# Optimization experiments

Hardware: AMD Instinct MI355X
Metric: run time of the kernel (lower is better)

The kernel has to match this reference:

```python
import jax, jax.numpy as jnp
import numpy as np

N, F, H, T = 100000, 128, 128, 10
E = 1600000
NUM_GRAPHS = 512
BN_EPS = 1e-5


def setup_inputs() -> dict:
    key = jax.random.key(0)
    ks = jax.random.split(key, 16)
    x = jax.random.normal(ks[0], (N, F), dtype=jnp.float32)
    edge_index = jax.random.randint(ks[1], (2, E), 0, N, dtype=jnp.int64)
    batch = jnp.sort(jax.random.randint(ks[2], (N,), 0, NUM_GRAPHS, dtype=jnp.int64))
    s = lambda fin: 1.0 / np.sqrt(fin)
    return {
        "x": x, "edge_index": edge_index, "batch": batch,
        # GINConv 1 MLP: Linear(F,H) -> BN(H) -> ReLU -> Linear(H,H)
        "W1a": jax.random.uniform(ks[3], (F, H), jnp.float32, -s(F), s(F)),
        "b1a": jax.random.uniform(ks[4], (H,), jnp.float32, -s(F), s(F)),
        "g1": jnp.ones((H,), jnp.float32),
        "bt1": jnp.zeros((H,), jnp.float32),
        "W1b": jax.random.uniform(ks[5], (H, H), jnp.float32, -s(H), s(H)),
        "b1b": jax.random.uniform(ks[6], (H,), jnp.float32, -s(H), s(H)),
        # GINConv 2 MLP
        "W2a": jax.random.uniform(ks[7], (H, H), jnp.float32, -s(H), s(H)),
        "b2a": jax.random.uniform(ks[8], (H,), jnp.float32, -s(H), s(H)),
        "g2": jnp.ones((H,), jnp.float32),
        "bt2": jnp.zeros((H,), jnp.float32),
        "W2b": jax.random.uniform(ks[9], (H, H), jnp.float32, -s(H), s(H)),
        "b2b": jax.random.uniform(ks[10], (H,), jnp.float32, -s(H), s(H)),
        # final Linear(H, T)
        "Wl": jax.random.uniform(ks[11], (H, T), jnp.float32, -s(H), s(H)),
        "bl": jax.random.uniform(ks[12], (T,), jnp.float32, -s(H), s(H)),
    }


def _batchnorm(h, gamma, beta):
    # training-mode BN over the node dimension (biased variance), eps=1e-5
    mean = jnp.mean(h, axis=0)
    var = jnp.mean(jnp.square(h - mean), axis=0)
    return (h - mean) * jax.lax.rsqrt(var + BN_EPS) * gamma + beta


def _gin_conv(x, edge_index, Wa, ba, gamma, beta, Wb, bb):
    src, dst = edge_index[0], edge_index[1]
    # sum-aggregate neighbor messages: scatter-add x[src] into dst rows
    agg = jax.ops.segment_sum(x[src], dst, num_segments=x.shape[0])
    h = (x + agg) @ Wa + ba          # eps=0 in GINConv default
    h = jax.nn.relu(_batchnorm(h, gamma, beta))
    return h @ Wb + bb


def reference(x, edge_index, batch, W1a, b1a, g1, bt1, W1b, b1b,
              W2a, b2a, g2, bt2, W2b, b2b, Wl, bl):
    h = jax.nn.relu(_gin_conv(x, edge_index, W1a, b1a, g1, bt1, W1b, b1b))
    h = jax.nn.relu(_gin_conv(h, edge_index, W2a, b2a, g2, bt2, W2b, b2b))
    pooled = jax.ops.segment_sum(h, batch, num_segments=NUM_GRAPHS)  # [G, H]
    return pooled @ Wl + bl  # [G, T]
```

## Files before the change

kernel.cpp:

```cpp
#include <hip/hip_runtime.h>
#include <cstdint>
#include <cstddef>

#define NFEAT 128
#define TGRAPH 10
#define NGRAPHS 512
#define BN_EPS 1e-5f
#define BIN_CHUNK 2048
#define GSPAN 8
#define TSTR 24

typedef __attribute__((ext_vector_type(8))) short bf16x8;
typedef __attribute__((ext_vector_type(4))) float f32x4;
typedef __attribute__((ext_vector_type(2))) float f32x2;

__device__ __forceinline__ float bf2f(short s) {
    union { unsigned u; float f; } c;
    c.u = ((unsigned)(unsigned short)s) << 16;
    return c.f;
}
__device__ __forceinline__ short f2bf(float f) {
    union { float f; unsigned u; } c;
    c.f = f;
    unsigned u = c.u;
    return (short)((u + 0x7fffu + ((u >> 16) & 1u)) >> 16);
}
__device__ __forceinline__ unsigned cvt_pk_bf16(float lo, float hi) {
    unsigned r;
    asm("v_cvt_pk_bf16_f32 %0, %1, %2" : "=v"(r) : "v"(lo), "v"(hi));
    return r;
}
__device__ __forceinline__ void accp(f32x2& a, unsigned v) {
    union { unsigned u; float f; } lo, hi;
    lo.u = v << 16;
    hi.u = v & 0xffff0000u;
    f32x2 t;
    t[0] = lo.f;
    t[1] = hi.f;
    a += t;
}


__global__ void k_bucket_scan(const int* __restrict__ bhist, int* __restrict__ bbase,
                              int* __restrict__ cur256, int E) {
    __shared__ int s[256];
    int t = threadIdx.x;
    int v = bhist[t];
    s[t] = v;
    __syncthreads();
    for (int off = 1; off < 256; off <<= 1) {
        int x = 0;
        if (t >= off) x = s[t - off];
        __syncthreads();
        if (t >= off) s[t] += x;
        __syncthreads();
    }
    int excl = s[t] - v;
    bbase[t] = excl;
    cur256[t] = excl;
    if (t == 255) bbase[256] = E;
}

__global__ __launch_bounds__(256) void k_bin_scatter(const int* __restrict__ src,
                                                     const int* __restrict__ dst,
                                                     int* __restrict__ cur256,
                                                     int2* __restrict__ binned, int E) {
    __shared__ int hist[256];
    __shared__ int base[256];
    int t = threadIdx.x;
    int e0 = blockIdx.x * BIN_CHUNK;
    int e1 = min(e0 + BIN_CHUNK, E);
    hist[t] = 0;
    __syncthreads();
    for (int e = e0 + t; e < e1; e += 256) {
        int b = dst[e] >> 9;
        atomicAdd(&hist[b], 1);
    }
    __syncthreads();
    int c = hist[t];
    if (c > 0) base[t] = atomicAdd(&cur256[t], c);
    __syncthreads();
    hist[t] = 0;
    __syncthreads();
    for (int e = e0 + t; e < e1; e += 256) {
        int d = dst[e];
        int b = d >> 9;
        int loc = atomicAdd(&hist[b], 1);
        binned[base[b] + loc] = make_int2(src[e], d);
    }
}

__global__ __launch_bounds__(512) void k_bucket_csr(const int2* __restrict__ binned,
                                                    const int* __restrict__ bbase,
                                                    int* __restrict__ rowptr,
                                                    int* __restrict__ adj,
                                                    int N, int E, int nb) {
    __shared__ int deg[512];
    __shared__ int cur[512];
    int b = blockIdx.x;
    int t = threadIdx.x;
    int e0 = bbase[b], e1 = bbase[b + 1];
    deg[t] = 0;
    __syncthreads();
    for (int e = e0 + t; e < e1; e += 512)
        atomicAdd(&deg[binned[e].y & 511], 1);
    __syncthreads();
    int v = deg[t];
    for (int off = 1; off < 512; off <<= 1) {
        int x = 0;
        if (t >= off) x = deg[t - off];
        __syncthreads();
        if (t >= off) deg[t] += x;
        __syncthreads();
    }
    int excl = deg[t] - v;
    cur[t] = excl;
    int node = b * 512 + t;
    if (node < N) rowptr[node] = e0 + excl;
    if (b == nb - 1 && t == 0) rowptr[N] = E;
    __syncthreads();
    for (int e = e0 + t; e < e1; e += 512) {
        int2 p = binned[e];
        int loc = atomicAdd(&cur[p.y & 511], 1);
        adj[e0 + loc] = p.x;
    }
}

__global__ __launch_bounds__(256) void k_prep_hist(const int* __restrict__ dst,
                                                   int* __restrict__ bhist, int E, int hb,
                                                   const float* __restrict__ x,
                                                   short* __restrict__ xbf,
                                                   const float* __restrict__ W0,
                                                   const float* __restrict__ W1,
                                                   const float* __restrict__ W2,
                                                   const float* __restrict__ W3,
                                                   short* __restrict__ Wf, int n4) {
    int t = threadIdx.x;
    if (blockIdx.x < hb) {
        __shared__ int h[256];
        h[t] = 0;
        __syncthreads();
        for (int e = blockIdx.x * 256 + t; e < E; e += hb * 256)
            atomicAdd(&h[dst[e] >> 9], 1);
        __syncthreads();
        if (h[t]) atomicAdd(&bhist[t], h[t]);
        return;
    }
    int i = (blockIdx.x - hb) * 256 + t;
    if (i < n4) {
        float4 v = ((const float4*)x)[i];
        uint2 o;
        o.x = cvt_pk_bf16(v.x, v.y);
        o.y = cvt_pk_bf16(v.z, v.w);
        ((uint2*)xbf)[i] = o;
    } else {
        int idx = i - n4;
        if (idx < 4 * 16384) {
            int w = idx >> 14, r = idx & 16383;
            int j = r & 7, lane = (r >> 3) & 63, ct = (r >> 9) & 7, kc = r >> 12;
            int k = kc * 32 + (lane >> 4) * 8 + j;
            int n = ct * 16 + (lane & 15);
            const float* W = (w == 0) ? W0 : (w == 1) ? W1 : (w == 2) ? W2 : W3;
            Wf[idx] = f2bf(W[k * NFEAT + n]);
        }
    }
}

__global__ __launch_bounds__(256) void k_aggregate_v4(const short* __restrict__ X,
                                                      const int* __restrict__ rowptr,
                                                      const int* __restrict__ adj,
                                                      short* __restrict__ XA, int N) {
    int tid = threadIdx.x;
    int lane = tid & 63;
    int g = lane >> 4;
    int p = lane & 15;
    int wid = (blockIdx.x * blockDim.x + tid) >> 6;
    if (wid >= N) return;
    const uint4* Xv = (const uint4*)X;
    f32x2 ac[4];
#pragma unroll
    for (int j = 0; j < 4; j++) ac[j] = (f32x2){0.f, 0.f};
    int r0 = rowptr[wid], r1 = rowptr[wid + 1];
    for (int e = r0; e < r1; e += 16) {
        int ea = e + g, eb = e + 4 + g, ec = e + 8 + g, ed = e + 12 + g;
        uint4 v0 = {0u, 0u, 0u, 0u}, v1 = {0u, 0u, 0u, 0u};
        uint4 v2 = {0u, 0u, 0u, 0u}, v3 = {0u, 0u, 0u, 0u};
        if (ea < r1) v0 = Xv[(size_t)adj[ea] * 16 + p];
        if (eb < r1) v1 = Xv[(size_t)adj[eb] * 16 + p];
        if (ec < r1) v2 = Xv[(size_t)adj[ec] * 16 + p];
        if (ed < r1) v3 = Xv[(size_t)adj[ed] * 16 + p];
        accp(ac[0], v0.x); accp(ac[1], v0.y); accp(ac[2], v0.z); accp(ac[3], v0.w);
        accp(ac[0], v1.x); accp(ac[1], v1.y); accp(ac[2], v1.z); accp(ac[3], v1.w);
        accp(ac[0], v2.x); accp(ac[1], v2.y); accp(ac[2], v2.z); accp(ac[3], v2.w);
        accp(ac[0], v3.x); accp(ac[1], v3.y); accp(ac[2], v3.z); accp(ac[3], v3.w);
    }
#pragma unroll
    for (int j = 0; j < 4; j++) {
        ac[j][0] += __shfl_xor(ac[j][0], 16);
        ac[j][1] += __shfl_xor(ac[j][1], 16);
        ac[j][0] += __shfl_xor(ac[j][0], 32);
        ac[j][1] += __shfl_xor(ac[j][1], 32);
    }
    if (g == 0) {
        uint4 sv = Xv[(size_t)wid * 16 + p];
        accp(ac[0], sv.x); accp(ac[1], sv.y); accp(ac[2], sv.z); accp(ac[3], sv.w);
        uint4 o;
        o.x = cvt_pk_bf16(ac[0][0], ac[0][1]);
        o.y = cvt_pk_bf16(ac[1][0], ac[1][1]);
        o.z = cvt_pk_bf16(ac[2][0], ac[2][1]);
        o.w = cvt_pk_bf16(ac[3][0], ac[3][1]);
        size_t dst = ((size_t)(wid >> 4) * 4 + (p >> 2)) * 512 +
                     (size_t)(((p & 3) * 16 + (wid & 15)) * 8);
        *(uint4*)(XA + dst) = o;
    }
}

template <bool BN_RELU_IN, bool RELU_OUT, bool STATS, bool FRAG_OUT, bool POOL>
__global__ __launch_bounds__(256) void k_gemm_mfma(const short* __restrict__ A,
                                                   const short* __restrict__ Wf,
                                                   const float* __restrict__ bias,
                                                   float* __restrict__ stats,
                                                   const float* __restrict__ gamma,
                                                   const float* __restrict__ beta,
                                                   const int* __restrict__ batch,
                                                   float* __restrict__ pooled,
                                                   short* __restrict__ C, int N) {
    __shared__ float s_aux[256];
    __shared__ __align__(16) short c_tile[4][32 * TSTR];
    __shared__ float s_pool[GSPAN][NFEAT];
    int tid = threadIdx.x;
    int wave = tid >> 6, lane = tid & 63;
    int quad = lane >> 4, l16 = lane & 15;
    int row_base = blockIdx.x * 128 + wave * 32;

    int gbase = 0;
    if constexpr (POOL) {
        int first = blockIdx.x * 128;
        gbase = (first < N) ? batch[first] : 0;
        for (int i = tid; i < GSPAN * NFEAT; i += 256) s_pool[i >> 7][i & 127] = 0.f;
    }
    if constexpr (STATS) s_aux[tid] = 0.f;
    if constexpr (BN_RELU_IN) {
        if (tid < NFEAT) {
            float mean = stats[tid] / (float)N;
            float var = stats[NFEAT + tid] / (float)N - mean * mean;
            float inv = rsqrtf(var + BN_EPS);
            float sc = gamma[tid] * inv;
            s_aux[tid] = sc;
            s_aux[NFEAT + tid] = beta[tid] - mean * sc;
        }
    }
    if constexpr (STATS || BN_RELU_IN || POOL) __syncthreads();

    f32x4 acc[2][8];
#pragma unroll
    for (int i = 0; i < 2; i++)
#pragma unroll
        for (int j = 0; j < 8; j++) acc[i][j] = (f32x4){0.f, 0.f, 0.f, 0.f};

    const short* af = A + ((size_t)(blockIdx.x * 8 + wave * 2) * 4) * 512;

#pragma unroll
    for (int kc = 0; kc < 4; ++kc) {
        bf16x8 a0 = *(const bf16x8*)(af + (size_t)kc * 512 + lane * 8);
        bf16x8 a1 = *(const bf16x8*)(af + (size_t)(4 + kc) * 512 + lane * 8);
        if constexpr (BN_RELU_IN) {
            int koff = kc * 32 + quad * 8;
            union { bf16x8 v; unsigned u[4]; } r0, r1;
#pragma unroll
            for (int h = 0; h < 4; ++h) {
                float sca = s_aux[koff + 2 * h];
                float scb = s_aux[koff + 2 * h + 1];
                float sha = s_aux[NFEAT + koff + 2 * h];
                float shb = s_aux[NFEAT + koff + 2 * h + 1];
                float x0 = fmaxf(bf2f(a0[2 * h]) * sca + sha, 0.f);
                float x1 = fmaxf(bf2f(a0[2 * h + 1]) * scb + shb, 0.f);
                float y0 = fmaxf(bf2f(a1[2 * h]) * sca + sha, 0.f);
                float y1 = fmaxf(bf2f(a1[2 * h + 1]) * scb + shb, 0.f);
                r0.u[h] = cvt_pk_bf16(x0, x1);
                r1.u[h] = cvt_pk_bf16(y0, y1);
            }
            a0 = r0.v;
            a1 = r1.v;
        }
        const short* wp = Wf + ((size_t)(kc * 8) * 64 + lane) * 8;
#pragma unroll
        for (int ct = 0; ct < 8; ++ct) {
            bf16x8 b = *(const bf16x8*)(wp + (size_t)ct * 64 * 8);
            acc[0][ct] = __builtin_amdgcn_mfma_f32_16x16x32_bf16(a0, b, acc[0][ct], 0, 0, 0);
            acc[1][ct] = __builtin_amdgcn_mfma_f32_16x16x32_bf16(a1, b, acc[1][ct], 0, 0, 0);
        }
    }

    int dg[8];
    if constexpr (POOL) {
#pragma unroll
        for (int rt = 0; rt < 2; ++rt)
#pragma unroll
            for (int reg = 0; reg < 4; ++reg) {
                int row = row_base + rt * 16 + quad * 4 + reg;
                dg[rt * 4 + reg] = (row < N) ? (batch[row] - gbase) : -1;
            }
    }

    short* tile = &c_tile[wave][0];
    int row2 = lane >> 1, half = lane & 1;
#pragma unroll
    for (int ct = 0; ct < 8; ++ct) {
        int col = ct * 16 + l16;
        float bv = bias[col];
        float ls = 0.f, ls2 = 0.f;
        int cg = -1;
        float ps = 0.f;
#pragma unroll
        for (int rt = 0; rt < 2; ++rt) {
            float v[4];
#pragma unroll
            for (int reg = 0; reg < 4; ++reg) {
                int lrow = rt * 16 + quad * 4 + reg;
                float x = acc[rt][ct][reg] + bv;
                if constexpr (RELU_OUT) x = fmaxf(x, 0.f);
                if constexpr (STATS) {
                    if (row_base + lrow < N) { ls += x; ls2 += x * x; }
                }
                if constexpr (POOL) {
                    int d = dg[rt * 4 + reg];
                    if (d != cg) {
                        if (cg >= 0) atomicAdd(&s_pool[cg & (GSPAN - 1)][col], ps);
                        cg = d; ps = 0.f;
                    }
                    if (d >= 0) ps += x;
                }
                v[reg] = x;
            }
            if constexpr (!POOL) {
                unsigned p01 = cvt_pk_bf16(v[0], v[1]);
                unsigned p23 = cvt_pk_bf16(v[2], v[3]);
                int lr = rt * 16 + quad * 4;
                tile[lr * TSTR + l16] = (short)p01;
                tile[(lr + 1) * TSTR + l16] = (short)(p01 >> 16);
                tile[(lr + 2) * TSTR + l16] = (short)p23;
                tile[(lr + 3) * TSTR + l16] = (short)(p23 >> 16);
            }
        }
        if constexpr (POOL) {
            if (cg >= 0) atomicAdd(&s_pool[cg & (GSPAN - 1)][col], ps);
        }
        if constexpr (STATS) {
            ls += __shfl_xor(ls, 16);
            ls += __shfl_xor(ls, 32);
            ls2 += __shfl_xor(ls2, 16);
            ls2 += __shfl_xor(ls2, 32);
            if (quad == 0) {
                atomicAdd(&s_aux[col], ls);
                atomicAdd(&s_aux[NFEAT + col], ls2);
            }
        }
        if constexpr (!POOL) {
            uint4 val = *(const uint4*)(tile + row2 * TSTR + half * 8);
            int grow = row_base + row2;
            if (grow < N) {
                int col0 = ct * 16 + half * 8;
                if constexpr (FRAG_OUT) {
                    size_t addr = ((size_t)(grow >> 4) * 4 + (col0 >> 5)) * 512 +
                                  (size_t)((((col0 >> 3) & 3) * 16 + (grow & 15)) * 8);
                    *(uint4*)(C + addr) = val;
                } else {
                    *(uint4*)(C + (size_t)grow * NFEAT + col0) = val;
                }
            }
        }
    }

    if constexpr (STATS) {
        __syncthreads();
        if (tid < NFEAT) {
            atomicAdd(&stats[tid], s_aux[tid]);
            atomicAdd(&stats[NFEAT + tid], s_aux[NFEAT + tid]);
        }
    }
    if constexpr (POOL) {
        __syncthreads();
        for (int i = tid; i < GSPAN * NFEAT; i += 256) {
            float v = s_pool[i >> 7][i & 127];
            if (v != 0.f) {
                int gg = gbase + (i >> 7);
                if (gg < NGRAPHS) atomicAdd(&pooled[gg * NFEAT + (i & 127)], v);
            }
        }
    }
}

__global__ void k_final(const float* __restrict__ pooled, const float* __restrict__ Wl,
                        const float* __restrict__ bl, float* __restrict__ out) {
    int idx = blockIdx.x * blockDim.x + threadIdx.x;
    if (idx >= NGRAPHS * TGRAPH) return;
    int g = idx / TGRAPH, t = idx % TGRAPH;
    const float* p = pooled + (size_t)g * NFEAT;
    float acc = bl[t];
#pragma unroll 16
    for (int k = 0; k < NFEAT; ++k) acc += p[k] * Wl[k * TGRAPH + t];
    out[idx] = acc;
}

extern "C" void kernel_launch(void* const* d_in, const int* in_sizes, int n_in,
                              void* d_out, int out_size, void* d_ws, size_t ws_size,
                              hipStream_t stream) {
    const float* x = (const float*)d_in[0];
    const int* ei = (const int*)d_in[1];
    const int* batch = (const int*)d_in[2];
    const float* W1a = (const float*)d_in[3];
    const float* b1a = (const float*)d_in[4];
    const float* g1 = (const float*)d_in[5];
    const float* bt1 = (const float*)d_in[6];
    const float* W1b = (const float*)d_in[7];
    const float* b1b = (const float*)d_in[8];
    const float* W2a = (const float*)d_in[9];
    const float* b2a = (const float*)d_in[10];
    const float* g2 = (const float*)d_in[11];
    const float* bt2 = (const float*)d_in[12];
    const float* W2b = (const float*)d_in[13];
    const float* b2b = (const float*)d_in[14];
    const float* Wl = (const float*)d_in[15];
    const float* bl = (const float*)d_in[16];
    float* out = (float*)d_out;

    int N = in_sizes[2];
    int E = in_sizes[1] / 2;
    int nb = (N + 511) >> 9;
    const int* src = ei;
    const int* dst = ei + E;

    int gemmBlocks = (N + 127) / 128;
    int padRows = gemmBlocks * 128;

    char* ws = (char*)d_ws;
    size_t off = 0;
    auto alloc = [&](size_t bytes) -> void* {
        void* p = ws + off;
        off = (off + bytes + 255) & ~(size_t)255;
        return p;
    };
    short* xbf = (short*)alloc((size_t)N * NFEAT * 2);
    short* ag = (short*)alloc((size_t)padRows * NFEAT * 2);
    short* ybf = (short*)alloc((size_t)padRows * NFEAT * 2);
    short* hbf = (short*)alloc((size_t)N * NFEAT * 2);
    short* Wf = (short*)alloc((size_t)4 * 16384 * 2);
    int* adj = (int*)alloc((size_t)E * 4);
    int2* binned = (int2*)alloc((size_t)E * 8);
    int* rowptr = (int*)alloc((size_t)(N + 1) * 4);
    int* bbase = (int*)alloc(257 * 4);
    int* cur256 = (int*)alloc(256 * 4);
    int* bhist = (int*)alloc(256 * 4);
    float* stats1 = (float*)alloc(256 * 4);
    float* stats2 = (float*)alloc(256 * 4);
    float* pooled = (float*)alloc((size_t)NGRAPHS * NFEAT * 4);
    size_t zbytes = (char*)(pooled + (size_t)NGRAPHS * NFEAT) - (char*)bhist;

    hipMemsetAsync(bhist, 0, zbytes, stream);

    int n4 = N * NFEAT / 4;
    int prepTot = n4 + 4 * 16384;
    int hb = 784;
    k_prep_hist<<<hb + (prepTot + 255) / 256, 256, 0, stream>>>(
        dst, bhist, E, hb, x, xbf, W1a, W1b, W2a, W2b, Wf, n4);
    k_bucket_scan<<<1, 256, 0, stream>>>(bhist, bbase, cur256, E);
    k_bin_scatter<<<(E + BIN_CHUNK - 1) / BIN_CHUNK, 256, 0, stream>>>(src, dst, cur256, binned, E);
    k_bucket_csr<<<nb, 512, 0, stream>>>(binned, bbase, rowptr, adj, N, E, nb);

    int aggBlocks = (N + 3) / 4;

    k_aggregate_v4<<<aggBlocks, 256, 0, stream>>>(xbf, rowptr, adj, ag, N);
    k_gemm_mfma<false, false, true, true, false><<<gemmBlocks, 256, 0, stream>>>(
        ag, Wf + 0 * 16384, b1a, stats1, nullptr, nullptr, nullptr, nullptr, ybf, N);
    k_gemm_mfma<true, true, false, false, false><<<gemmBlocks, 256, 0, stream>>>(
        ybf, Wf + 1 * 16384, b1b, stats1, g1, bt1, nullptr, nullptr, hbf, N);

    k_aggregate_v4<<<aggBlocks, 256, 0, stream>>>(hbf, rowptr, adj, ag, N);
    k_gemm_mfma<false, false, true, true, false><<<gemmBlocks, 256, 0, stream>>>(
        ag, Wf + 2 * 16384, b2a, stats2, nullptr, nullptr, nullptr, nullptr, ybf, N);
    k_gemm_mfma<true, true, false, false, true><<<gemmBlocks, 256, 0, stream>>>(
        ybf, Wf + 3 * 16384, b2b, stats2, g2, bt2, batch, pooled, nullptr, N);

    k_final<<<(NGRAPHS * TGRAPH + 255) / 256, 256, 0, stream>>>(pooled, Wl, bl, out);
}
```

Baseline: 449.5 us.

## Fuse both GIN MLP GEMMs into one persistent kernel with grid barrier

The two GEMMs of each GIN MLP, split before by the BatchNorm statistics dependency, now run in one persistent kernel sized to occupancy. A software grid barrier on an atomic counter sits between the two phases. Each block keeps its first 128-row intermediate tile in LDS, so part of the Y write and reread through global memory is skipped, and one launch per layer is removed. The cost is a spin barrier that deadlocks if not all blocks are co-resident, extra LDS use that limits occupancy, and fewer blocks each looping over several tiles.

```diff
diff --git a/kernel.cpp b/kernel.cpp
--- a/kernel.cpp
+++ b/kernel.cpp
@@ -215,125 +215,69 @@
     }
 }
 
-template <bool BN_RELU_IN, bool RELU_OUT, bool STATS, bool FRAG_OUT, bool POOL>
-__global__ __launch_bounds__(256) void k_gemm_mfma(const short* __restrict__ A,
-                                                   const short* __restrict__ Wf,
-                                                   const float* __restrict__ bias,
-                                                   float* __restrict__ stats,
-                                                   const float* __restrict__ gamma,
-                                                   const float* __restrict__ beta,
-                                                   const int* __restrict__ batch,
-                                                   float* __restrict__ pooled,
-                                                   short* __restrict__ C, int N) {
+template <bool POOLB>
+__global__ __launch_bounds__(256, 3) void k_gemm_fused(
+    const short* __restrict__ A, const short* __restrict__ Wa,
+    const short* __restrict__ Wb, const float* __restrict__ ba,
+    const float* __restrict__ bb, float* __restrict__ stats,
+    const float* __restrict__ gamma, const float* __restrict__ beta,
+    const int* __restrict__ batch, float* __restrict__ pooled,
+    short* __restrict__ Y, short* __restrict__ C,
+    int* __restrict__ bar, int nTiles, int N) {
     __shared__ float s_aux[256];
+    __shared__ __align__(16) short ylds[16384];
     __shared__ __align__(16) short c_tile[4][32 * TSTR];
     __shared__ float s_pool[GSPAN][NFEAT];
     int tid = threadIdx.x;
     int wave = tid >> 6, lane = tid & 63;
     int quad = lane >> 4, l16 = lane & 15;
-    int row_base = blockIdx.x * 128 + wave * 32;
-
-    int gbase = 0;
-    if constexpr (POOL) {
-        int first = blockIdx.x * 128;
-        gbase = (first < N) ? batch[first] : 0;
-        for (int i = tid; i < GSPAN * NFEAT; i += 256) s_pool[i >> 7][i & 127] = 0.f;
-    }
-    if constexpr (STATS) s_aux[tid] = 0.f;
-    if constexpr (BN_RELU_IN) {
-        if (tid < NFEAT) {
-            float mean = stats[tid] / (float)N;
-            float var = stats[NFEAT + tid] / (float)N - mean * mean;
-            float inv = rsqrtf(var + BN_EPS);
-            float sc = gamma[tid] * inv;
-            s_aux[tid] = sc;
-            s_aux[NFEAT + tid] = beta[tid] - mean * sc;
-        }
-    }
-    if constexpr (STATS || BN_RELU_IN || POOL) __syncthreads();
-
-    f32x4 acc[2][8];
-#pragma unroll
-    for (int i = 0; i < 2; i++)
-#pragma unroll
-        for (int j = 0; j < 8; j++) acc[i][j] = (f32x4){0.f, 0.f, 0.f, 0.f};
-
-    const short* af = A + ((size_t)(blockIdx.x * 8 + wave * 2) * 4) * 512;
-
-#pragma unroll
-    for (int kc = 0; kc < 4; ++kc) {
-        bf16x8 a0 = *(const bf16x8*)(af + (size_t)kc * 512 + lane * 8);
-        bf16x8 a1 = *(const bf16x8*)(af + (size_t)(4 + kc) * 512 + lane * 8);
-        if constexpr (BN_RELU_IN) {
-            int koff = kc * 32 + quad * 8;
-            union { bf16x8 v; unsigned u[4]; } r0, r1;
-#pragma unroll
-            for (int h = 0; h < 4; ++h) {
-                float sca = s_aux[koff + 2 * h];
-                float scb = s_aux[koff + 2 * h + 1];
-                float sha = s_aux[NFEAT + koff + 2 * h];
-                float shb = s_aux[NFEAT + koff + 2 * h + 1];
-                float x0 = fmaxf(bf2f(a0[2 * h]) * sca + sha, 0.f);
-                float x1 = fmaxf(bf2f(a0[2 * h + 1]) * scb + shb, 0.f);
-                float y0 = fmaxf(bf2f(a1[2 * h]) * sca + sha, 0.f);
-                float y1 = fmaxf(bf2f(a1[2 * h + 1]) * scb + shb, 0.f);
-                r0.u[h] = cvt_pk_bf16(x0, x1);
-                r1.u[h] = cvt_pk_bf16(y0, y1);
-            }
-            a0 = r0.v;
-            a1 = r1.v;
-        }
-        const short* wp = Wf + ((size_t)(kc * 8) * 64 + lane) * 8;
+    int row2 = lane >> 1, half = lane & 1;
+
+    bool lds0 = true;
+    for (int t = blockIdx.x; t < nTiles; t += gridDim.x, lds0 = false) {
+        int row_base = t * 128 + wave * 32;
+        const short* af = A + ((size_t)(t * 8 + wave * 2) * 4) * 512;
+        bf16x8 a0[4], a1[4];
+#pragma unroll
+        for (int kc = 0; kc < 4; ++kc) {
+            a0[kc] = *(const bf16x8*)(af + (size_t)kc * 512 + lane * 8);
+            a1[kc] = *(const bf16x8*)(af + (size_t)(4 + kc) * 512 + lane * 8);
+        }
+        s_aux[tid] = 0.f;
+        __syncthreads();
+
+        f32x4 acc[2][8];
+#pragma unroll
+        for (int i = 0; i < 2; i++)
+#pragma unroll
+            for (int j = 0; j < 8; j++) acc[i][j] = (f32x4){0.f, 0.f, 0.f, 0.f};
+#pragma unroll
+        for (int kc = 0; kc < 4; ++kc) {
+            const short* wp = Wa + ((size_t)(kc * 8) * 64 + lane) * 8;
+#pragma unroll
+            for (int ct = 0; ct < 8; ++ct) {
+                bf16x8 b = *(const bf16x8*)(wp + (size_t)ct * 64 * 8);
+                acc[0][ct] = __builtin_amdgcn_mfma_f32_16x16x32_bf16(a0[kc], b, acc[0][ct], 0, 0, 0);
+                acc[1][ct] = __builtin_amdgcn_mfma_f32_16x16x32_bf16(a1[kc], b, acc[1][ct], 0, 0, 0);
+            }
+        }
+
+        short* tile = &c_tile[wave][0];
 #pragma unroll
         for (int ct = 0; ct < 8; ++ct) {
-            bf16x8 b = *(const bf16x8*)(wp + (size_t)ct * 64 * 8);
-            acc[0][ct] = __builtin_amdgcn_mfma_f32_16x16x32_bf16(a0, b, acc[0][ct], 0, 0, 0);
-            acc[1][ct] = __builtin_amdgcn_mfma_f32_16x16x32_bf16(a1, b, acc[1][ct], 0, 0, 0);
-        }
-    }
-
-    int dg[8];
-    if constexpr (POOL) {
-#pragma unroll
-        for (int rt = 0; rt < 2; ++rt)
-#pragma unroll
-            for (int reg = 0; reg < 4; ++reg) {
-                int row = row_base + rt * 16 + quad * 4 + reg;
-                dg[rt * 4 + reg] = (row < N) ? (batch[row] - gbase) : -1;
-            }
-    }
-
-    short* tile = &c_tile[wave][0];
-    int row2 = lane >> 1, half = lane & 1;
-#pragma unroll
-    for (int ct = 0; ct < 8; ++ct) {
-        int col = ct * 16 + l16;
-        float bv = bias[col];
-        float ls = 0.f, ls2 = 0.f;
-        int cg = -1;
-        float ps = 0.f;
-#pragma unroll
-        for (int rt = 0; rt < 2; ++rt) {
-            float v[4];
-#pragma unroll
-            for (int reg = 0; reg < 4; ++reg) {
-                int lrow = rt * 16 + quad * 4 + reg;
-                float x = acc[rt][ct][reg] + bv;
-                if constexpr (RELU_OUT) x = fmaxf(x, 0.f);
-                if constexpr (STATS) {
+            int col = ct * 16 + l16;
+            float bv = ba[col];
+            float ls = 0.f, ls2 = 0.f;
+#pragma unroll
+            for (int rt = 0; rt < 2; ++rt) {
+                float v[4];
+#pragma unroll
+                for (int reg = 0; reg < 4; ++reg) {
+                    int lrow = rt * 16 + quad * 4 + reg;
+                    float x = acc[rt][ct][reg] + bv;
                     if (row_base + lrow < N) { ls += x; ls2 += x * x; }
+                    v[reg] = x;
                 }
-                if constexpr (POOL) {
-                    int d = dg[rt * 4 + reg];
-                    if (d != cg) {
-                        if (cg >= 0) atomicAdd(&s_pool[cg & (GSPAN - 1)][col], ps);
-                        cg = d; ps = 0.f;
-                    }
-                    if (d >= 0) ps += x;
-                }
-                v[reg] = x;
-            }
-            if constexpr (!POOL) {
                 unsigned p01 = cvt_pk_bf16(v[0], v[1]);
                 unsigned p23 = cvt_pk_bf16(v[2], v[3]);
                 int lr = rt * 16 + quad * 4;
@@ -342,11 +286,6 @@
                 tile[(lr + 2) * TSTR + l16] = (short)p23;
                 tile[(lr + 3) * TSTR + l16] = (short)(p23 >> 16);
             }
-        }
-        if constexpr (POOL) {
-            if (cg >= 0) atomicAdd(&s_pool[cg & (GSPAN - 1)][col], ps);
-        }
-        if constexpr (STATS) {
             ls += __shfl_xor(ls, 16);
             ls += __shfl_xor(ls, 32);
             ls2 += __shfl_xor(ls2, 16);
@@ -355,37 +294,168 @@
                 atomicAdd(&s_aux[col], ls);
                 atomicAdd(&s_aux[NFEAT + col], ls2);
             }
-        }
-        if constexpr (!POOL) {
             uint4 val = *(const uint4*)(tile + row2 * TSTR + half * 8);
-            int grow = row_base + row2;
-            if (grow < N) {
-                int col0 = ct * 16 + half * 8;
-                if constexpr (FRAG_OUT) {
-                    size_t addr = ((size_t)(grow >> 4) * 4 + (col0 >> 5)) * 512 +
-                                  (size_t)((((col0 >> 3) & 3) * 16 + (grow & 15)) * 8);
-                    *(uint4*)(C + addr) = val;
-                } else {
-                    *(uint4*)(C + (size_t)grow * NFEAT + col0) = val;
-                }
-            }
-        }
-    }
-
-    if constexpr (STATS) {
+            int lrow2 = wave * 32 + row2;
+            int col0 = ct * 16 + half * 8;
+            size_t fa = ((size_t)(lrow2 >> 4) * 4 + (col0 >> 5)) * 512 +
+                        (size_t)((((col0 >> 3) & 3) * 16 + (lrow2 & 15)) * 8);
+            if (lds0) {
+                *(uint4*)(ylds + fa) = val;
+            } else {
+                int grow = row_base + row2;
+                if (grow < N) *(uint4*)(Y + (size_t)t * 16384 + fa) = val;
+            }
+        }
         __syncthreads();
         if (tid < NFEAT) {
             atomicAdd(&stats[tid], s_aux[tid]);
             atomicAdd(&stats[NFEAT + tid], s_aux[NFEAT + tid]);
         }
-    }
-    if constexpr (POOL) {
-        __syncthreads();
-        for (int i = tid; i < GSPAN * NFEAT; i += 256) {
-            float v = s_pool[i >> 7][i & 127];
-            if (v != 0.f) {
-                int gg = gbase + (i >> 7);
-                if (gg < NGRAPHS) atomicAdd(&pooled[gg * NFEAT + (i & 127)], v);
+        __syncthreads();
+    }
+
+    __threadfence();
+    __syncthreads();
+    if (tid == 0) {
+        __hip_atomic_fetch_add(bar, 1, __ATOMIC_RELEASE, __HIP_MEMORY_SCOPE_AGENT);
+        while (__hip_atomic_load(bar, __ATOMIC_ACQUIRE, __HIP_MEMORY_SCOPE_AGENT) < (int)gridDim.x)
+            __builtin_amdgcn_s_sleep(8);
+    }
+    __syncthreads();
+    __threadfence();
+
+    if (tid < NFEAT) {
+        float sum = __hip_atomic_load(&stats[tid], __ATOMIC_RELAXED, __HIP_MEMORY_SCOPE_AGENT);
+        float sq = __hip_atomic_load(&stats[NFEAT + tid], __ATOMIC_RELAXED, __HIP_MEMORY_SCOPE_AGENT);
+        float mean = sum / (float)N;
+        float var = sq / (float)N - mean * mean;
+        float inv = rsqrtf(var + BN_EPS);
+        float sc = gamma[tid] * inv;
+        s_aux[tid] = sc;
+        s_aux[NFEAT + tid] = beta[tid] - mean * sc;
+    }
+    __syncthreads();
+
+    lds0 = true;
+    for (int t = blockIdx.x; t < nTiles; t += gridDim.x, lds0 = false) {
+        int row_base = t * 128 + wave * 32;
+        bf16x8 a0[4], a1[4];
+        if (lds0) {
+            const short* af = ylds + (size_t)(wave * 2 * 4) * 512;
+#pragma unroll
+            for (int kc = 0; kc < 4; ++kc) {
+                a0[kc] = *(const bf16x8*)(af + (size_t)kc * 512 + lane * 8);
+                a1[kc] = *(const bf16x8*)(af + (size_t)(4 + kc) * 512 + lane * 8);
+            }
+        } else {
+            const short* af = Y + (size_t)t * 16384 + (size_t)(wave * 2 * 4) * 512;
+#pragma unroll
+            for (int kc = 0; kc < 4; ++kc) {
+                a0[kc] = *(const bf16x8*)(af + (size_t)kc * 512 + lane * 8);
+                a1[kc] = *(const bf16x8*)(af + (size_t)(4 + kc) * 512 + lane * 8);
+            }
+        }
+        int gbase = 0;
+        if constexpr (POOLB) {
+            gbase = batch[t * 128];
+            for (int i = tid; i < GSPAN * NFEAT; i += 256) s_pool[i >> 7][i & 127] = 0.f;
+            __syncthreads();
+        }
+
+        f32x4 acc[2][8];
+#pragma unroll
+        for (int i = 0; i < 2; i++)
+#pragma unroll
+            for (int j = 0; j < 8; j++) acc[i][j] = (f32x4){0.f, 0.f, 0.f, 0.f};
+#pragma unroll
+        for (int kc = 0; kc < 4; ++kc) {
+            int koff = kc * 32 + quad * 8;
+            union { bf16x8 v; unsigned u[4]; } r0, r1;
+#pragma unroll
+            for (int h = 0; h < 4; ++h) {
+                float sca = s_aux[koff + 2 * h];
+                float scb = s_aux[koff + 2 * h + 1];
+                float sha = s_aux[NFEAT + koff + 2 * h];
+                float shb = s_aux[NFEAT + koff + 2 * h + 1];
+                float x0 = fmaxf(bf2f(a0[kc][2 * h]) * sca + sha, 0.f);
+                float x1 = fmaxf(bf2f(a0[kc][2 * h + 1]) * scb + shb, 0.f);
+                float y0 = fmaxf(bf2f(a1[kc][2 * h]) * sca + sha, 0.f);
+                float y1 = fmaxf(bf2f(a1[kc][2 * h + 1]) * scb + shb, 0.f);
+                r0.u[h] = cvt_pk_bf16(x0, x1);
+                r1.u[h] = cvt_pk_bf16(y0, y1);
+            }
+            const short* wp = Wb + ((size_t)(kc * 8) * 64 + lane) * 8;
+#pragma unroll
+            for (int ct = 0; ct < 8; ++ct) {
+                bf16x8 b = *(const bf16x8*)(wp + (size_t)ct * 64 * 8);
+                acc[0][ct] = __builtin_amdgcn_mfma_f32_16x16x32_bf16(r0.v, b, acc[0][ct], 0, 0, 0);
+                acc[1][ct] = __builtin_amdgcn_mfma_f32_16x16x32_bf16(r1.v, b, acc[1][ct], 0, 0, 0);
+            }
+        }
+
+        int dg[8];
+        if constexpr (POOLB) {
+#pragma unroll
+            for (int rt = 0; rt < 2; ++rt)
+#pragma unroll
+                for (int reg = 0; reg < 4; ++reg) {
+                    int row = row_base + rt * 16 + quad * 4 + reg;
+                    dg[rt * 4 + reg] = (row < N) ? (batch[row] - gbase) : -1;
+                }
+        }
+
+        short* tile = &c_tile[wave][0];
+#pragma unroll
+        for (int ct = 0; ct < 8; ++ct) {
+            int col = ct * 16 + l16;
+            float bv = bb[col];
+            int cg = -1;
+            float ps = 0.f;
+#pragma unroll
+            for (int rt = 0; rt < 2; ++rt) {
+                float v[4];
+#pragma unroll
+                for (int reg = 0; reg < 4; ++reg) {
+                    float x = fmaxf(acc[rt][ct][reg] + bv, 0.f);
+                    if constexpr (POOLB) {
+                        int d = dg[rt * 4 + reg];
+                        if (d != cg) {
+                            if (cg >= 0) atomicAdd(&s_pool[cg & (GSPAN - 1)][col], ps);
+                            cg = d; ps = 0.f;
+                        }
+                        if (d >= 0) ps += x;
+                    }
+                    v[reg] = x;
+                }
+                if constexpr (!POOLB) {
+                    unsigned p01 = cvt_pk_bf16(v[0], v[1]);
+                    unsigned p23 = cvt_pk_bf16(v[2], v[3]);
+                    int lr = rt * 16 + quad * 4;
+                    tile[lr * TSTR + l16] = (short)p01;
+                    tile[(lr + 1) * TSTR + l16] = (short)(p01 >> 16);
+                    tile[(lr + 2) * TSTR + l16] = (short)p23;
+                    tile[(lr + 3) * TSTR + l16] = (short)(p23 >> 16);
+                }
+            }
+            if constexpr (POOLB) {
+                if (cg >= 0) atomicAdd(&s_pool[cg & (GSPAN - 1)][col], ps);
+            } else {
+                uint4 val = *(const uint4*)(tile + row2 * TSTR + half * 8);
+                int grow = row_base + row2;
+                if (grow < N) {
+                    int col0 = ct * 16 + half * 8;
+                    *(uint4*)(C + (size_t)grow * NFEAT + col0) = val;
+                }
+            }
+        }
+        if constexpr (POOLB) {
+            __syncthreads();
+            for (int i = tid; i < GSPAN * NFEAT; i += 256) {
+                float v = s_pool[i >> 7][i & 127];
+                if (v != 0.f) {
+                    int gg = gbase + (i >> 7);
+                    if (gg < NGRAPHS) atomicAdd(&pooled[gg * NFEAT + (i & 127)], v);
+                }
             }
         }
     }
@@ -431,8 +501,17 @@
     const int* src = ei;
     const int* dst = ei + E;
 
-    int gemmBlocks = (N + 127) / 128;
-    int padRows = gemmBlocks * 128;
+    int nTiles = (N + 127) / 128;
+    int padRows = nTiles * 128;
+
+    int occ1 = 0, occ2 = 0;
+    hipOccupancyMaxActiveBlocksPerMultiprocessor(&occ1, k_gemm_fused<false>, 256, 0);
+    hipOccupancyMaxActiveBlocksPerMultiprocessor(&occ2, k_gemm_fused<true>, 256, 0);
+    int occ = occ1 < occ2 ? occ1 : occ2;
+    if (occ < 1) occ = 1;
+    if (occ > 3) occ = 3;
+    int G = occ * 256;
+    if (G > nTiles) G = nTiles;
 
     char* ws = (char*)d_ws;
     size_t off = 0;
@@ -454,6 +533,8 @@
     int* bhist = (int*)alloc(256 * 4);
     float* stats1 = (float*)alloc(256 * 4);
     float* stats2 = (float*)alloc(256 * 4);
+    int* bar1 = (int*)alloc(256);
+    int* bar2 = (int*)alloc(256);
     float* pooled = (float*)alloc((size_t)NGRAPHS * NFEAT * 4);
     size_t zbytes = (char*)(pooled + (size_t)NGRAPHS * NFEAT) - (char*)bhist;
 
@@ -471,16 +552,14 @@
     int aggBlocks = (N + 3) / 4;
 
     k_aggregate_v4<<<aggBlocks, 256, 0, stream>>>(xbf, rowptr, adj, ag, N);
-    k_gemm_mfma<false, false, true, true, false><<<gemmBlocks, 256, 0, stream>>>(
-        ag, Wf + 0 * 16384, b1a, stats1, nullptr, nullptr, nullptr, nullptr, ybf, N);
-    k_gemm_mfma<true, true, false, false, false><<<gemmBlocks, 256, 0, stream>>>(
-        ybf, Wf + 1 * 16384, b1b, stats1, g1, bt1, nullptr, nullptr, hbf, N);
+    k_gemm_fused<false><<<G, 256, 0, stream>>>(ag, Wf + 0 * 16384, Wf + 1 * 16384, b1a, b1b,
+                                               stats1, g1, bt1, nullptr, nullptr, ybf, hbf,
+                                               bar1, nTiles, N);
 
     k_aggregate_v4<<<aggBlocks, 256, 0, stream>>>(hbf, rowptr, adj, ag, N);
-    k_gemm_mfma<false, false, true, true, false><<<gemmBlocks, 256, 0, stream>>>(
-        ag, Wf + 2 * 16384, b2a, stats2, nullptr, nullptr, nullptr, nullptr, ybf, N);
-    k_gemm_mfma<true, true, false, false, true><<<gemmBlocks, 256, 0, stream>>>(
-        ybf, Wf + 3 * 16384, b2b, stats2, g2, bt2, batch, pooled, nullptr, N);
+    k_gemm_fused<true><<<G, 256, 0, stream>>>(ag, Wf + 2 * 16384, Wf + 3 * 16384, b2a, b2b,
+                                              stats2, g2, bt2, batch, pooled, ybf, nullptr,
+                                              bar2, nTiles, N);
 
     k_final<<<(NGRAPHS * TGRAPH + 255) / 256, 256, 0, stream>>>(pooled, Wl, bl, out);
 }
```

After: 652.7 us. 1.45x slower.
